# Kernel optimization log

Hardware: AMD Instinct MI355X
Metric: run time of the kernel (lower is better)

Reference implementation:

```python
import jax, jax.numpy as jnp
import numpy as np

N = 100000       # num_nodes
E = 800000       # num edges (avg degree 8)
EMB = 64         # emb_dim
HID = 256        # hidden_dim


def setup_inputs() -> dict:
    key = jax.random.key(0)
    k1, k2, k3, k4, k5, k6, k7 = jax.random.split(key, 7)
    def xavier(k, fan_in, fan_out):
        limit = float(np.sqrt(6.0 / (fan_in + fan_out)))
        return jax.random.uniform(k, (fan_in, fan_out), jnp.float32, -limit, limit)
    return {
        "row": jax.random.randint(k1, (E,), 0, N, dtype=jnp.int64) if jax.config.jax_enable_x64 else jax.random.randint(k1, (E,), 0, N).astype(jnp.int32),
        "col": jax.random.randint(k2, (E,), 0, N).astype(jnp.int32),
        "val": jax.random.uniform(k3, (E,), jnp.float32),
        "emb": jax.random.normal(k4, (N, EMB), jnp.float32) * 0.02,
        "W0": xavier(k5, EMB, HID),
        "W1": xavier(k6, HID, HID),
        "W2": xavier(k7, HID, HID),
    }


def reference(row, col, val, emb, W0, W1, W2):
    # SpMM: out[r] = sum_{edges e with row[e]==r} val[e] * emb[col[e]]
    msgs = val[:, None] * emb[col]                      # [E, EMB] gather + scale
    x = jax.ops.segment_sum(msgs, row, num_segments=N)  # [N, EMB] scatter-add
    # MLP (bias-free linears; dropout=0.0 / eval mode => identity)
    x = jax.nn.relu(x @ W0)   # [N, HID]
    x = jax.nn.relu(x @ W1)   # [N, HID]
    x = x @ W2                # [N, HID]
    return x
```

## Files before the change

### kernel.cpp

```cpp
#include <hip/hip_runtime.h>
#include <hip/hip_bf16.h>

#define EMB 64
#define HID 256

typedef __attribute__((ext_vector_type(8))) short short8_t;
typedef __attribute__((ext_vector_type(4))) float f32x4;

__device__ __forceinline__ unsigned short f2bf(float f)
{
    union { float f; unsigned int u; } c; c.f = f;
    unsigned int u = c.u;
    u += 0x7fffu + ((u >> 16) & 1u);
    return (unsigned short)(u >> 16);
}
__device__ __forceinline__ float bf2f(unsigned short b)
{
    union { unsigned int u; float f; } c; c.u = ((unsigned int)b) << 16;
    return c.f;
}

__global__ __launch_bounds__(256) void prep_kernel(
    const float* __restrict__ emb, const float* __restrict__ W0,
    const float* __restrict__ W1, const float* __restrict__ W2,
    int* __restrict__ counts, unsigned short* __restrict__ embb,
    unsigned short* __restrict__ W0t, unsigned short* __restrict__ W1t,
    unsigned short* __restrict__ W2t, int M, int zb, int cb)
{
    int b = blockIdx.x;
    if (b < zb) {
        int idx = (b * 256 + threadIdx.x) * 4;
        if (idx + 3 < M) {
            int4 z; z.x = 0; z.y = 0; z.z = 0; z.w = 0;
            *(int4*)&counts[idx] = z;
        } else {
            for (int i = idx; i < M; ++i) counts[i] = 0;
        }
        return;
    }
    b -= zb;
    if (b < cb) {
        int idx = (b * 256 + threadIdx.x) * 4;
        if (idx + 3 < M * EMB) {
            float4 v = *(const float4*)&emb[idx];
            ushort4 o;
            o.x = f2bf(v.x); o.y = f2bf(v.y); o.z = f2bf(v.z); o.w = f2bf(v.w);
            *(ushort4*)&embb[idx] = o;
        }
        return;
    }
    b -= cb;
    if (b < EMB) {
        int i = b * 256 + threadIdx.x;
        int k = i >> 8, n = i & 255;
        W0t[n * EMB + k] = f2bf(W0[i]);
        return;
    }
    b -= EMB;
    if (b < HID) {
        int i = b * 256 + threadIdx.x;
        int k = i >> 8, n = i & 255;
        W1t[n * HID + k] = f2bf(W1[i]);
        return;
    }
    b -= HID;
    {
        int i = b * 256 + threadIdx.x;
        int k = i >> 8, n = i & 255;
        W2t[n * HID + k] = f2bf(W2[i]);
    }
}

__global__ __launch_bounds__(256) void hist_kernel(
    const int* __restrict__ row, int* __restrict__ counts, int E)
{
    int base = (blockIdx.x * 256 + threadIdx.x) * 4;
    if (base + 3 < E) {
        int4 r4 = *(const int4*)&row[base];
        atomicAdd(&counts[r4.x], 1);
        atomicAdd(&counts[r4.y], 1);
        atomicAdd(&counts[r4.z], 1);
        atomicAdd(&counts[r4.w], 1);
    } else {
        for (int i = base; i < E; ++i) atomicAdd(&counts[row[i]], 1);
    }
}

__global__ __launch_bounds__(256) void scan_phase1(
    const int* __restrict__ counts, int* __restrict__ excl,
    int* __restrict__ blockSums, int n)
{
    __shared__ int s[256];
    int t = threadIdx.x;
    int base = blockIdx.x * 1024 + t * 4;
    int4 v = {0, 0, 0, 0};
    if (base + 3 < n) {
        v = *(const int4*)&counts[base];
    } else {
        if (base + 0 < n) v.x = counts[base + 0];
        if (base + 1 < n) v.y = counts[base + 1];
        if (base + 2 < n) v.z = counts[base + 2];
        if (base + 3 < n) v.w = counts[base + 3];
    }
    int tsum = v.x + v.y + v.z + v.w;
    s[t] = tsum;
    __syncthreads();
#pragma unroll
    for (int off = 1; off < 256; off <<= 1) {
        int val = (t >= off) ? s[t - off] : 0;
        __syncthreads();
        s[t] += val;
        __syncthreads();
    }
    if (t == 255) blockSums[blockIdx.x] = s[255];
    int e0 = s[t] - tsum;
    int e1 = e0 + v.x;
    int e2 = e1 + v.y;
    int e3 = e2 + v.z;
    if (base + 0 < n) excl[base + 0] = e0;
    if (base + 1 < n) excl[base + 1] = e1;
    if (base + 2 < n) excl[base + 2] = e2;
    if (base + 3 < n) excl[base + 3] = e3;
}

__global__ __launch_bounds__(256) void scan_phase2(int* blockSums, int nb)
{
    __shared__ int s[256];
    int t = threadIdx.x;
    int v = (t < nb) ? blockSums[t] : 0;
    s[t] = v;
    __syncthreads();
#pragma unroll
    for (int off = 1; off < 256; off <<= 1) {
        int val = (t >= off) ? s[t - off] : 0;
        __syncthreads();
        s[t] += val;
        __syncthreads();
    }
    if (t < nb) blockSums[t] = s[t] - v;
}

__global__ __launch_bounds__(256) void scan_phase3(
    int* __restrict__ offsets, const int* __restrict__ blockSums,
    int* __restrict__ cursor, int n)
{
    int i = blockIdx.x * 256 + threadIdx.x;
    if (i >= n) return;
    int o = offsets[i] + blockSums[i >> 10];
    offsets[i] = o;
    cursor[i]  = o;
}

__global__ __launch_bounds__(256) void scatter_kernel(
    const int* __restrict__ row, const int* __restrict__ col,
    const float* __restrict__ val, int* __restrict__ cursor,
    uint2* __restrict__ edata, int E)
{
    int e = blockIdx.x * 256 + threadIdx.x;
    if (e >= E) return;
    int r = row[e];
    int pos = atomicAdd(&cursor[r], 1);
    uint2 d;
    d.x = (unsigned)col[e];
    d.y = __float_as_uint(val[e]);
    edata[pos] = d;
}

__global__ __launch_bounds__(256) void pull_kernel(
    const int* __restrict__ offsets, const int* __restrict__ counts,
    const uint2* __restrict__ edata, const unsigned short* __restrict__ embb,
    unsigned short* __restrict__ xb, int Nn)
{
    int r    = blockIdx.x * 4 + (threadIdx.x >> 6);
    int lane = threadIdx.x & 63;
    if (r >= Nn) return;
    int beg = offsets[r];
    int cnt = counts[r];
    float acc = 0.f;
    for (int i = 0; i < cnt; i += 8) {
        uint2 ed[8];
#pragma unroll
        for (int j = 0; j < 8; ++j) {
            int idx = i + j;
            idx = (idx < cnt) ? idx : (cnt - 1);
            ed[j] = edata[beg + idx];
        }
        float g[8];
#pragma unroll
        for (int j = 0; j < 8; ++j)
            g[j] = bf2f(embb[(size_t)ed[j].x * EMB + lane]);
#pragma unroll
        for (int j = 0; j < 8; ++j) {
            float v = (i + j < cnt) ? __uint_as_float(ed[j].y) : 0.f;
            acc += v * g[j];
        }
    }
    xb[(size_t)r * EMB + lane] = f2bf(acc);
}

__global__ __launch_bounds__(256) void mlp_fused(
    const unsigned short* __restrict__ xb,
    const unsigned short* __restrict__ W0t,
    const unsigned short* __restrict__ W1t,
    const unsigned short* __restrict__ W2t,
    float* __restrict__ out, int M)
{
    constexpr int LDK = 72;
    constexpr int LDH = 264;
    __shared__ unsigned short As[64 * LDK];
    __shared__ unsigned short Bs[256 * LDK];
    __shared__ unsigned short H [64 * LDH];

    const int t    = threadIdx.x;
    const int lane = t & 63;
    const int w    = t >> 6;
    const int lr   = lane & 15;
    const int kg   = lane >> 4;
    const int row0 = blockIdx.x * 64;

#pragma unroll
    for (int c = 0; c < 2; ++c) {
        int chunk = t + c * 256;
        int r = chunk >> 3, ko = (chunk & 7) * 8;
        int gr = row0 + r;
        *(short8_t*)&As[r * LDK + ko] =
            *(const short8_t*)(xb + (size_t)(gr < M ? gr : 0) * EMB + ko);
    }
#pragma unroll
    for (int c = 0; c < 8; ++c) {
        int chunk = t + c * 256;
        int n = chunk >> 3, ko = (chunk & 7) * 8;
        *(short8_t*)&Bs[n * LDK + ko] = *(const short8_t*)(W0t + n * EMB + ko);
    }
    __syncthreads();

    f32x4 acc[4][4] = {};
#pragma unroll
    for (int ks = 0; ks < 64; ks += 32) {
        short8_t a[4], b[4];
#pragma unroll
        for (int m = 0; m < 4; ++m)
            a[m] = *(const short8_t*)&As[(m * 16 + lr) * LDK + ks + kg * 8];
#pragma unroll
        for (int n = 0; n < 4; ++n)
            b[n] = *(const short8_t*)&Bs[(w * 64 + n * 16 + lr) * LDK + ks + kg * 8];
#pragma unroll
        for (int m = 0; m < 4; ++m)
#pragma unroll
            for (int n = 0; n < 4; ++n)
                acc[m][n] = __builtin_amdgcn_mfma_f32_16x16x32_bf16(
                    a[m], b[n], acc[m][n], 0, 0, 0);
    }
#pragma unroll
    for (int m = 0; m < 4; ++m)
#pragma unroll
        for (int r = 0; r < 4; ++r)
#pragma unroll
            for (int n = 0; n < 4; ++n)
                H[(m * 16 + kg * 4 + r) * LDH + w * 64 + n * 16 + lr] =
                    f2bf(fmaxf(acc[m][n][r], 0.f));
    __syncthreads();

    f32x4 acc2[4][4] = {};
    for (int k0 = 0; k0 < HID; k0 += 64) {
#pragma unroll
        for (int c = 0; c < 8; ++c) {
            int chunk = t + c * 256;
            int n = chunk >> 3, ko = (chunk & 7) * 8;
            *(short8_t*)&Bs[n * LDK + ko] =
                *(const short8_t*)(W1t + (size_t)n * HID + k0 + ko);
        }
        __syncthreads();
#pragma unroll
        for (int ks = 0; ks < 64; ks += 32) {
            short8_t a[4], b[4];
#pragma unroll
            for (int m = 0; m < 4; ++m)
                a[m] = *(const short8_t*)&H[(m * 16 + lr) * LDH + k0 + ks + kg * 8];
#pragma unroll
            for (int n = 0; n < 4; ++n)
                b[n] = *(const short8_t*)&Bs[(w * 64 + n * 16 + lr) * LDK + ks + kg * 8];
#pragma unroll
            for (int m = 0; m < 4; ++m)
#pragma unroll
                for (int n = 0; n < 4; ++n)
                    acc2[m][n] = __builtin_amdgcn_mfma_f32_16x16x32_bf16(
                        a[m], b[n], acc2[m][n], 0, 0, 0);
        }
        __syncthreads();
    }
#pragma unroll
    for (int m = 0; m < 4; ++m)
#pragma unroll
        for (int r = 0; r < 4; ++r)
#pragma unroll
            for (int n = 0; n < 4; ++n)
                H[(m * 16 + kg * 4 + r) * LDH + w * 64 + n * 16 + lr] =
                    f2bf(fmaxf(acc2[m][n][r], 0.f));

    f32x4 acc3[4][4] = {};
    for (int k0 = 0; k0 < HID; k0 += 64) {
#pragma unroll
        for (int c = 0; c < 8; ++c) {
            int chunk = t + c * 256;
            int n = chunk >> 3, ko = (chunk & 7) * 8;
            *(short8_t*)&Bs[n * LDK + ko] =
                *(const short8_t*)(W2t + (size_t)n * HID + k0 + ko);
        }
        __syncthreads();
#pragma unroll
        for (int ks = 0; ks < 64; ks += 32) {
            short8_t a[4], b[4];
#pragma unroll
            for (int m = 0; m < 4; ++m)
                a[m] = *(const short8_t*)&H[(m * 16 + lr) * LDH + k0 + ks + kg * 8];
#pragma unroll
            for (int n = 0; n < 4; ++n)
                b[n] = *(const short8_t*)&Bs[(w * 64 + n * 16 + lr) * LDK + ks + kg * 8];
#pragma unroll
            for (int m = 0; m < 4; ++m)
#pragma unroll
                for (int n = 0; n < 4; ++n)
                    acc3[m][n] = __builtin_amdgcn_mfma_f32_16x16x32_bf16(
                        a[m], b[n], acc3[m][n], 0, 0, 0);
        }
        __syncthreads();
    }
#pragma unroll
    for (int m = 0; m < 4; ++m)
#pragma unroll
        for (int r = 0; r < 4; ++r) {
            int gr = row0 + m * 16 + kg * 4 + r;
            if (gr < M)
#pragma unroll
                for (int n = 0; n < 4; ++n)
                    out[(size_t)gr * HID + w * 64 + n * 16 + lr] = acc3[m][n][r];
        }
}

__global__ __launch_bounds__(256) void spmm_kernel(
    const int* __restrict__ row, const int* __restrict__ col,
    const float* __restrict__ val, const float* __restrict__ emb,
    float* __restrict__ x, int E)
{
    int gid  = blockIdx.x * blockDim.x + threadIdx.x;
    int e    = gid >> 6;
    int lane = gid & 63;
    if (e >= E) return;
    unsafeAtomicAdd(&x[(size_t)row[e] * EMB + lane],
                    val[e] * emb[(size_t)col[e] * EMB + lane]);
}

template<int K, bool RELU>
__global__ __launch_bounds__(256) void gemm_f32(
    const float* A, const float* __restrict__ B, float* C, int M)
{
    __shared__ float As[64][17];
    __shared__ float Bs[16][256];

    const int t    = threadIdx.x;
    const int tn   = t & 15;
    const int row0 = blockIdx.x * 64;
    const int sk = t & 15;
    const int sm = (t >> 4) * 4;

    float acc[4][16];
#pragma unroll
    for (int i = 0; i < 4; ++i)
#pragma unroll
        for (int j = 0; j < 16; ++j) acc[i][j] = 0.f;

    const int mB = ((t & 63) >> 4) * 4;
    const int wq = t >> 6;
    const int myM = (wq * 16) + mB;

    for (int k0 = 0; k0 < K; k0 += 16) {
        __syncthreads();
#pragma unroll
        for (int i = 0; i < 4; ++i) {
            int m  = sm + i;
            int gr = row0 + m;
            As[m][sk] = (gr < M) ? A[(size_t)gr * K + k0 + sk] : 0.f;
        }
#pragma unroll
        for (int r = 0; r < 16; ++r)
            Bs[r][t] = B[(size_t)(k0 + r) * 256 + t];
        __syncthreads();

#pragma unroll
        for (int kk = 0; kk < 16; ++kk) {
            float a0 = As[myM + 0][kk];
            float a1 = As[myM + 1][kk];
            float a2 = As[myM + 2][kk];
            float a3 = As[myM + 3][kk];
            float4 b[4];
#pragma unroll
            for (int j = 0; j < 4; ++j)
                b[j] = *(const float4*)&Bs[kk][tn * 4 + j * 64];
#pragma unroll
            for (int j = 0; j < 4; ++j) {
                acc[0][j*4+0] += a0 * b[j].x;  acc[0][j*4+1] += a0 * b[j].y;
                acc[0][j*4+2] += a0 * b[j].z;  acc[0][j*4+3] += a0 * b[j].w;
                acc[1][j*4+0] += a1 * b[j].x;  acc[1][j*4+1] += a1 * b[j].y;
                acc[1][j*4+2] += a1 * b[j].z;  acc[1][j*4+3] += a1 * b[j].w;
                acc[2][j*4+0] += a2 * b[j].x;  acc[2][j*4+1] += a2 * b[j].y;
                acc[2][j*4+2] += a2 * b[j].z;  acc[2][j*4+3] += a2 * b[j].w;
                acc[3][j*4+0] += a3 * b[j].x;  acc[3][j*4+1] += a3 * b[j].y;
                acc[3][j*4+2] += a3 * b[j].z;  acc[3][j*4+3] += a3 * b[j].w;
            }
        }
    }

#pragma unroll
    for (int i = 0; i < 4; ++i) {
        int gr = row0 + myM + i;
        if (gr < M) {
#pragma unroll
            for (int j = 0; j < 4; ++j) {
                float4 o;
                o.x = acc[i][j*4+0]; o.y = acc[i][j*4+1];
                o.z = acc[i][j*4+2]; o.w = acc[i][j*4+3];
                if (RELU) {
                    o.x = fmaxf(o.x, 0.f); o.y = fmaxf(o.y, 0.f);
                    o.z = fmaxf(o.z, 0.f); o.w = fmaxf(o.w, 0.f);
                }
                *(float4*)&C[(size_t)gr * 256 + tn * 4 + j * 64] = o;
            }
        }
    }
}

extern "C" void kernel_launch(void* const* d_in, const int* in_sizes, int n_in,
                              void* d_out, int out_size, void* d_ws, size_t ws_size,
                              hipStream_t stream)
{
    const int*   row = (const int*)d_in[0];
    const int*   col = (const int*)d_in[1];
    const float* val = (const float*)d_in[2];
    const float* emb = (const float*)d_in[3];
    const float* W0  = (const float*)d_in[4];
    const float* W1  = (const float*)d_in[5];
    const float* W2  = (const float*)d_in[6];
    float* out = (float*)d_out;

    const int E = in_sizes[0];
    const int M = in_sizes[3] / EMB;

    char* ws = (char*)d_ws;

    size_t off = 0;
    auto alloc = [&](size_t bytes) { size_t o = off; off = (off + bytes + 255) & ~(size_t)255; return o; };
    const size_t off_counts = alloc((size_t)M * 4);
    const size_t off_offs   = alloc((size_t)M * 4);
    const size_t off_cursor = alloc((size_t)M * 4);
    const size_t off_bsums  = alloc(1024);
    const size_t off_edata  = alloc((size_t)E * 8);
    const size_t off_embb   = alloc((size_t)M * EMB * 2);
    const size_t off_xb     = alloc((size_t)M * EMB * 2);
    const size_t off_w0     = alloc((size_t)EMB * HID * 2);
    const size_t off_w1     = alloc((size_t)HID * HID * 2);
    const size_t off_w2     = alloc((size_t)HID * HID * 2);
    const size_t need       = off;

    int gblocks = (M + 63) / 64;

    if (ws_size >= need) {
        int*   counts = (int*)(ws + off_counts);
        int*   offs   = (int*)(ws + off_offs);
        int*   cursor = (int*)(ws + off_cursor);
        int*   bsums  = (int*)(ws + off_bsums);
        uint2* edata  = (uint2*)(ws + off_edata);
        unsigned short* embb = (unsigned short*)(ws + off_embb);
        unsigned short* xb  = (unsigned short*)(ws + off_xb);
        unsigned short* W0t = (unsigned short*)(ws + off_w0);
        unsigned short* W1t = (unsigned short*)(ws + off_w1);
        unsigned short* W2t = (unsigned short*)(ws + off_w2);

        int zb = (M / 4 + 255) / 256;
        int cb = ((M * EMB) / 4 + 255) / 256;
        int prep_blocks = zb + cb + EMB + HID + HID;
        prep_kernel<<<prep_blocks, 256, 0, stream>>>(
            emb, W0, W1, W2, counts, embb, W0t, W1t, W2t, M, zb, cb);

        hist_kernel<<<(E / 4 + 255) / 256, 256, 0, stream>>>(row, counts, E);
        int nb = (M + 1023) / 1024;
        scan_phase1<<<nb, 256, 0, stream>>>(counts, offs, bsums, M);
        scan_phase2<<<1, 256, 0, stream>>>(bsums, nb);
        scan_phase3<<<(M + 255) / 256, 256, 0, stream>>>(offs, bsums, cursor, M);
        scatter_kernel<<<(E + 255) / 256, 256, 0, stream>>>(row, col, val, cursor, edata, E);

        pull_kernel<<<(M + 3) / 4, 256, 0, stream>>>(offs, counts, edata, embb, xb, M);

        mlp_fused<<<gblocks, 256, 0, stream>>>(xb, W0t, W1t, W2t, out, M);
    } else {
        float* x = (float*)ws;
        (void)hipMemsetAsync(x, 0, (size_t)M * EMB * sizeof(float), stream);
        spmm_kernel<<<(E + 3) / 4, 256, 0, stream>>>(row, col, val, emb, x, E);
        gemm_f32<EMB, true ><<<gblocks, 256, 0, stream>>>(x,   W0, out, M);
        gemm_f32<HID, true ><<<gblocks, 256, 0, stream>>>(out, W1, out, M);
        gemm_f32<HID, false><<<gblocks, 256, 0, stream>>>(out, W2, out, M);
    }
}
```

Before: 203.6 us.

## Double-buffer weight tiles with register prefetch in fused MLP kernel

Restructures the fused three-layer MLP kernel to stage weight K-slices of 32 through two shared-memory buffers, with global loads prefetched into registers one step ahead. This overlaps weight fetches with MFMA work and halves the barriers per K step. The input activations are loaded straight into registers, so the As tile goes away. Shared memory use drops, which may allow more blocks per CU, at the cost of more live registers for the prefetch staging.

```diff
diff --git a/kernel.cpp b/kernel.cpp
--- a/kernel.cpp
+++ b/kernel.cpp
@@ -205,10 +205,9 @@
     const unsigned short* __restrict__ W2t,
     float* __restrict__ out, int M)
 {
-    constexpr int LDK = 72;
+    constexpr int LDK = 40;
     constexpr int LDH = 264;
-    __shared__ unsigned short As[64 * LDK];
-    __shared__ unsigned short Bs[256 * LDK];
+    __shared__ unsigned short Bs[2][256 * LDK];
     __shared__ unsigned short H [64 * LDH];
 
     const int t    = threadIdx.x;
@@ -218,38 +217,52 @@
     const int kg   = lane >> 4;
     const int row0 = blockIdx.x * 64;
 
-#pragma unroll
-    for (int c = 0; c < 2; ++c) {
-        int chunk = t + c * 256;
-        int r = chunk >> 3, ko = (chunk & 7) * 8;
-        int gr = row0 + r;
-        *(short8_t*)&As[r * LDK + ko] =
-            *(const short8_t*)(xb + (size_t)(gr < M ? gr : 0) * EMB + ko);
-    }
-#pragma unroll
-    for (int c = 0; c < 8; ++c) {
-        int chunk = t + c * 256;
-        int n = chunk >> 3, ko = (chunk & 7) * 8;
-        *(short8_t*)&Bs[n * LDK + ko] = *(const short8_t*)(W0t + n * EMB + ko);
-    }
+    const int srow = t >> 2;
+    const int sq   = (t & 3) * 8;
+
+    short8_t st[4];
+#define LOADC(src, ldk, k0)                                                    \
+    do {                                                                       \
+        _Pragma("unroll")                                                      \
+        for (int c = 0; c < 4; ++c)                                            \
+            st[c] = *(const short8_t*)((src) + (size_t)(64 * c + srow) * (ldk) \
+                                       + (k0) + sq);                           \
+    } while (0)
+#define WRITEC(buf)                                                            \
+    do {                                                                       \
+        _Pragma("unroll")                                                      \
+        for (int c = 0; c < 4; ++c)                                            \
+            *(short8_t*)&Bs[buf][(64 * c + srow) * LDK + sq] = st[c];          \
+    } while (0)
+
+    short8_t ax[2][4];
+#pragma unroll
+    for (int h = 0; h < 2; ++h)
+#pragma unroll
+        for (int m = 0; m < 4; ++m) {
+            int gr = row0 + m * 16 + lr;
+            ax[h][m] = *(const short8_t*)(xb + (size_t)(gr < M ? gr : 0) * EMB
+                                          + h * 32 + kg * 8);
+        }
+
+    LOADC(W0t, EMB, 0);  WRITEC(0);
+    LOADC(W0t, EMB, 32); WRITEC(1);
     __syncthreads();
+    LOADC(W1t, HID, 0);
 
     f32x4 acc[4][4] = {};
 #pragma unroll
-    for (int ks = 0; ks < 64; ks += 32) {
-        short8_t a[4], b[4];
-#pragma unroll
-        for (int m = 0; m < 4; ++m)
-            a[m] = *(const short8_t*)&As[(m * 16 + lr) * LDK + ks + kg * 8];
+    for (int h = 0; h < 2; ++h) {
+        short8_t b[4];
 #pragma unroll
         for (int n = 0; n < 4; ++n)
-            b[n] = *(const short8_t*)&Bs[(w * 64 + n * 16 + lr) * LDK + ks + kg * 8];
+            b[n] = *(const short8_t*)&Bs[h][(w * 64 + n * 16 + lr) * LDK + kg * 8];
 #pragma unroll
         for (int m = 0; m < 4; ++m)
 #pragma unroll
             for (int n = 0; n < 4; ++n)
                 acc[m][n] = __builtin_amdgcn_mfma_f32_16x16x32_bf16(
-                    a[m], b[n], acc[m][n], 0, 0, 0);
+                    ax[h][m], b[n], acc[m][n], 0, 0, 0);
     }
 #pragma unroll
     for (int m = 0; m < 4; ++m)
@@ -261,31 +274,33 @@
                     f2bf(fmaxf(acc[m][n][r], 0.f));
     __syncthreads();
 
+    WRITEC(0);
+    LOADC(W1t, HID, 32);
+    __syncthreads();
+
     f32x4 acc2[4][4] = {};
-    for (int k0 = 0; k0 < HID; k0 += 64) {
-#pragma unroll
-        for (int c = 0; c < 8; ++c) {
-            int chunk = t + c * 256;
-            int n = chunk >> 3, ko = (chunk & 7) * 8;
-            *(short8_t*)&Bs[n * LDK + ko] =
-                *(const short8_t*)(W1t + (size_t)n * HID + k0 + ko);
-        }
-        __syncthreads();
-#pragma unroll
-        for (int ks = 0; ks < 64; ks += 32) {
-            short8_t a[4], b[4];
-#pragma unroll
-            for (int m = 0; m < 4; ++m)
-                a[m] = *(const short8_t*)&H[(m * 16 + lr) * LDH + k0 + ks + kg * 8];
+    for (int i = 0; i < 8; ++i) {
+        int cur = i & 1;
+        short8_t a[4], b[4];
+#pragma unroll
+        for (int m = 0; m < 4; ++m)
+            a[m] = *(const short8_t*)&H[(m * 16 + lr) * LDH + i * 32 + kg * 8];
+#pragma unroll
+        for (int n = 0; n < 4; ++n)
+            b[n] = *(const short8_t*)&Bs[cur][(w * 64 + n * 16 + lr) * LDK + kg * 8];
+#pragma unroll
+        for (int m = 0; m < 4; ++m)
 #pragma unroll
             for (int n = 0; n < 4; ++n)
-                b[n] = *(const short8_t*)&Bs[(w * 64 + n * 16 + lr) * LDK + ks + kg * 8];
-#pragma unroll
-            for (int m = 0; m < 4; ++m)
-#pragma unroll
-                for (int n = 0; n < 4; ++n)
-                    acc2[m][n] = __builtin_amdgcn_mfma_f32_16x16x32_bf16(
-                        a[m], b[n], acc2[m][n], 0, 0, 0);
+                acc2[m][n] = __builtin_amdgcn_mfma_f32_16x16x32_bf16(
+                    a[m], b[n], acc2[m][n], 0, 0, 0);
+        WRITEC(cur ^ 1);
+        if (i < 6) {
+            LOADC(W1t, HID, (i + 2) * 32);
+        } else if (i == 6) {
+            LOADC(W2t, HID, 0);
+        } else {
+            LOADC(W2t, HID, 32);
         }
         __syncthreads();
     }
@@ -297,34 +312,31 @@
             for (int n = 0; n < 4; ++n)
                 H[(m * 16 + kg * 4 + r) * LDH + w * 64 + n * 16 + lr] =
                     f2bf(fmaxf(acc2[m][n][r], 0.f));
+    __syncthreads();
 
     f32x4 acc3[4][4] = {};
-    for (int k0 = 0; k0 < HID; k0 += 64) {
-#pragma unroll
-        for (int c = 0; c < 8; ++c) {
-            int chunk = t + c * 256;
-            int n = chunk >> 3, ko = (chunk & 7) * 8;
-            *(short8_t*)&Bs[n * LDK + ko] =
-                *(const short8_t*)(W2t + (size_t)n * HID + k0 + ko);
-        }
-        __syncthreads();
-#pragma unroll
-        for (int ks = 0; ks < 64; ks += 32) {
-            short8_t a[4], b[4];
-#pragma unroll
-            for (int m = 0; m < 4; ++m)
-                a[m] = *(const short8_t*)&H[(m * 16 + lr) * LDH + k0 + ks + kg * 8];
+    for (int i = 0; i < 8; ++i) {
+        int cur = i & 1;
+        short8_t a[4], b[4];
+#pragma unroll
+        for (int m = 0; m < 4; ++m)
+            a[m] = *(const short8_t*)&H[(m * 16 + lr) * LDH + i * 32 + kg * 8];
+#pragma unroll
+        for (int n = 0; n < 4; ++n)
+            b[n] = *(const short8_t*)&Bs[cur][(w * 64 + n * 16 + lr) * LDK + kg * 8];
+#pragma unroll
+        for (int m = 0; m < 4; ++m)
 #pragma unroll
             for (int n = 0; n < 4; ++n)
-                b[n] = *(const short8_t*)&Bs[(w * 64 + n * 16 + lr) * LDK + ks + kg * 8];
-#pragma unroll
-            for (int m = 0; m < 4; ++m)
-#pragma unroll
-                for (int n = 0; n < 4; ++n)
-                    acc3[m][n] = __builtin_amdgcn_mfma_f32_16x16x32_bf16(
-                        a[m], b[n], acc3[m][n], 0, 0, 0);
-        }
-        __syncthreads();
+                acc3[m][n] = __builtin_amdgcn_mfma_f32_16x16x32_bf16(
+                    a[m], b[n], acc3[m][n], 0, 0, 0);
+        if (i < 7) {
+            WRITEC(cur ^ 1);
+            if (i < 6) {
+                LOADC(W2t, HID, (i + 2) * 32);
+            }
+            __syncthreads();
+        }
     }
 #pragma unroll
     for (int m = 0; m < 4; ++m)
@@ -336,6 +348,8 @@
                 for (int n = 0; n < 4; ++n)
                     out[(size_t)gr * HID + w * 64 + n * 16 + lr] = acc3[m][n][r];
         }
+#undef LOADC
+#undef WRITEC
 }
 
 __global__ __launch_bounds__(256) void spmm_kernel(
```

New measurement: 201.3 us. No clear change (-1.1%).

## Pre-swizzle weights into MFMA fragment order and read B operands straight from global

Applied to the files above, without the earlier changes.

The weight prep now writes W0/W1/W2 in per-lane MFMA fragment order, so the fused MLP loads B operands directly from global/L2 with one 16-byte load per lane and no longer stages them through shared memory. The first-layer A operand is also read directly from global into registers. The hidden activation buffer uses an XOR-swizzled unpadded layout to avoid LDS bank conflicts. Together these remove most __syncthreads and LDS traffic and cut LDS usage, which may raise occupancy, at the cost of every block re-reading weights from L2.

```diff
diff --git a/kernel.cpp b/kernel.cpp
--- a/kernel.cpp
+++ b/kernel.cpp
@@ -24,8 +24,8 @@
     const float* __restrict__ emb, const float* __restrict__ W0,
     const float* __restrict__ W1, const float* __restrict__ W2,
     int* __restrict__ counts, unsigned short* __restrict__ embb,
-    unsigned short* __restrict__ W0t, unsigned short* __restrict__ W1t,
-    unsigned short* __restrict__ W2t, int M, int zb, int cb)
+    unsigned short* __restrict__ W0f, unsigned short* __restrict__ W1f,
+    unsigned short* __restrict__ W2f, int M, int zb, int cb)
 {
     int b = blockIdx.x;
     if (b < zb) {
@@ -50,24 +50,45 @@
         return;
     }
     b -= cb;
-    if (b < EMB) {
-        int i = b * 256 + threadIdx.x;
-        int k = i >> 8, n = i & 255;
-        W0t[n * EMB + k] = f2bf(W0[i]);
+    if (b < 8) {
+        int i    = b * 256 + threadIdx.x;
+        int lane = i & 63;
+        int kc   = (i >> 6) & 1;
+        int nt   = i >> 7;
+        int lr   = lane & 15, kg = lane >> 4;
+        unsigned short tmp[8];
+#pragma unroll
+        for (int j = 0; j < 8; ++j)
+            tmp[j] = f2bf(W0[(kc * 32 + kg * 8 + j) * HID + nt * 16 + lr]);
+        *(short8_t*)&W0f[(size_t)i * 8] = *(short8_t*)tmp;
         return;
     }
-    b -= EMB;
-    if (b < HID) {
-        int i = b * 256 + threadIdx.x;
-        int k = i >> 8, n = i & 255;
-        W1t[n * HID + k] = f2bf(W1[i]);
+    b -= 8;
+    if (b < 32) {
+        int i    = b * 256 + threadIdx.x;
+        int lane = i & 63;
+        int kc   = (i >> 6) & 7;
+        int nt   = i >> 9;
+        int lr   = lane & 15, kg = lane >> 4;
+        unsigned short tmp[8];
+#pragma unroll
+        for (int j = 0; j < 8; ++j)
+            tmp[j] = f2bf(W1[(kc * 32 + kg * 8 + j) * HID + nt * 16 + lr]);
+        *(short8_t*)&W1f[(size_t)i * 8] = *(short8_t*)tmp;
         return;
     }
-    b -= HID;
+    b -= 32;
     {
-        int i = b * 256 + threadIdx.x;
-        int k = i >> 8, n = i & 255;
-        W2t[n * HID + k] = f2bf(W2[i]);
+        int i    = b * 256 + threadIdx.x;
+        int lane = i & 63;
+        int kc   = (i >> 6) & 7;
+        int nt   = i >> 9;
+        int lr   = lane & 15, kg = lane >> 4;
+        unsigned short tmp[8];
+#pragma unroll
+        for (int j = 0; j < 8; ++j)
+            tmp[j] = f2bf(W2[(kc * 32 + kg * 8 + j) * HID + nt * 16 + lr]);
+        *(short8_t*)&W2f[(size_t)i * 8] = *(short8_t*)tmp;
     }
 }
 
@@ -200,16 +221,12 @@
 
 __global__ __launch_bounds__(256) void mlp_fused(
     const unsigned short* __restrict__ xb,
-    const unsigned short* __restrict__ W0t,
-    const unsigned short* __restrict__ W1t,
-    const unsigned short* __restrict__ W2t,
+    const unsigned short* __restrict__ W0f,
+    const unsigned short* __restrict__ W1f,
+    const unsigned short* __restrict__ W2f,
     float* __restrict__ out, int M)
 {
-    constexpr int LDK = 72;
-    constexpr int LDH = 264;
-    __shared__ unsigned short As[64 * LDK];
-    __shared__ unsigned short Bs[256 * LDK];
-    __shared__ unsigned short H [64 * LDH];
+    __shared__ unsigned short H[64 * 256];
 
     const int t    = threadIdx.x;
     const int lane = t & 63;
@@ -217,39 +234,32 @@
     const int lr   = lane & 15;
     const int kg   = lane >> 4;
     const int row0 = blockIdx.x * 64;
-
-#pragma unroll
-    for (int c = 0; c < 2; ++c) {
-        int chunk = t + c * 256;
-        int r = chunk >> 3, ko = (chunk & 7) * 8;
-        int gr = row0 + r;
-        *(short8_t*)&As[r * LDK + ko] =
-            *(const short8_t*)(xb + (size_t)(gr < M ? gr : 0) * EMB + ko);
-    }
-#pragma unroll
-    for (int c = 0; c < 8; ++c) {
-        int chunk = t + c * 256;
-        int n = chunk >> 3, ko = (chunk & 7) * 8;
-        *(short8_t*)&Bs[n * LDK + ko] = *(const short8_t*)(W0t + n * EMB + ko);
-    }
-    __syncthreads();
-
+    char* Hb = (char*)H;
+
+#define HOFF(row, bytecol) ((((row) * 512) + (bytecol)) ^ (((row) & 7) << 4))
+
+    short8_t ax[2][4];
+#pragma unroll
+    for (int kc = 0; kc < 2; ++kc)
+#pragma unroll
+        for (int m = 0; m < 4; ++m) {
+            int gr = row0 + m * 16 + lr;
+            ax[kc][m] = *(const short8_t*)(xb + (size_t)(gr < M ? gr : 0) * EMB
+                                           + kc * 32 + kg * 8);
+        }
     f32x4 acc[4][4] = {};
 #pragma unroll
-    for (int ks = 0; ks < 64; ks += 32) {
-        short8_t a[4], b[4];
-#pragma unroll
-        for (int m = 0; m < 4; ++m)
-            a[m] = *(const short8_t*)&As[(m * 16 + lr) * LDK + ks + kg * 8];
+    for (int kc = 0; kc < 2; ++kc) {
+        short8_t b[4];
 #pragma unroll
         for (int n = 0; n < 4; ++n)
-            b[n] = *(const short8_t*)&Bs[(w * 64 + n * 16 + lr) * LDK + ks + kg * 8];
+            b[n] = *(const short8_t*)&W0f[(size_t)(((w * 4 + n) * 2 + kc) * 64 + lane) * 8];
 #pragma unroll
         for (int m = 0; m < 4; ++m)
 #pragma unroll
             for (int n = 0; n < 4; ++n)
                 acc[m][n] = __builtin_amdgcn_mfma_f32_16x16x32_bf16(
-                    a[m], b[n], acc[m][n], 0, 0, 0);
+                    ax[kc][m], b[n], acc[m][n], 0, 0, 0);
     }
 #pragma unroll
     for (int m = 0; m < 4; ++m)
@@ -257,74 +267,56 @@
         for (int r = 0; r < 4; ++r)
 #pragma unroll
             for (int n = 0; n < 4; ++n)
-                H[(m * 16 + kg * 4 + r) * LDH + w * 64 + n * 16 + lr] =
+                *(unsigned short*)(Hb + HOFF(m * 16 + kg * 4 + r,
+                                             (w * 64 + n * 16 + lr) * 2)) =
                     f2bf(fmaxf(acc[m][n][r], 0.f));
     __syncthreads();
 
     f32x4 acc2[4][4] = {};
-    for (int k0 = 0; k0 < HID; k0 += 64) {
-#pragma unroll
-        for (int c = 0; c < 8; ++c) {
-            int chunk = t + c * 256;
-            int n = chunk >> 3, ko = (chunk & 7) * 8;
-            *(short8_t*)&Bs[n * LDK + ko] =
-                *(const short8_t*)(W1t + (size_t)n * HID + k0 + ko);
-        }
-        __syncthreads();
-#pragma unroll
-        for (int ks = 0; ks < 64; ks += 32) {
-            short8_t a[4], b[4];
-#pragma unroll
-            for (int m = 0; m < 4; ++m)
-                a[m] = *(const short8_t*)&H[(m * 16 + lr) * LDH + k0 + ks + kg * 8];
+#pragma unroll
+    for (int kc = 0; kc < 8; ++kc) {
+        short8_t a[4], b[4];
+#pragma unroll
+        for (int n = 0; n < 4; ++n)
+            b[n] = *(const short8_t*)&W1f[(size_t)(((w * 4 + n) * 8 + kc) * 64 + lane) * 8];
+#pragma unroll
+        for (int m = 0; m < 4; ++m)
+            a[m] = *(const short8_t*)(Hb + HOFF(m * 16 + lr, kc * 64 + kg * 16));
+#pragma unroll
+        for (int m = 0; m < 4; ++m)
 #pragma unroll
             for (int n = 0; n < 4; ++n)
-                b[n] = *(const short8_t*)&Bs[(w * 64 + n * 16 + lr) * LDK + ks + kg * 8];
-#pragma unroll
-            for (int m = 0; m < 4; ++m)
-#pragma unroll
-                for (int n = 0; n < 4; ++n)
-                    acc2[m][n] = __builtin_amdgcn_mfma_f32_16x16x32_bf16(
-                        a[m], b[n], acc2[m][n], 0, 0, 0);
-        }
-        __syncthreads();
-    }
+                acc2[m][n] = __builtin_amdgcn_mfma_f32_16x16x32_bf16(
+                    a[m], b[n], acc2[m][n], 0, 0, 0);
+    }
+    __syncthreads();
 #pragma unroll
     for (int m = 0; m < 4; ++m)
 #pragma unroll
         for (int r = 0; r < 4; ++r)
 #pragma unroll
             for (int n = 0; n < 4; ++n)
-                H[(m * 16 + kg * 4 + r) * LDH + w * 64 + n * 16 + lr] =
+                *(unsigned short*)(Hb + HOFF(m * 16 + kg * 4 + r,
+                                             (w * 64 + n * 16 + lr) * 2)) =
                     f2bf(fmaxf(acc2[m][n][r], 0.f));
+    __syncthreads();
 
     f32x4 acc3[4][4] = {};
-    for (int k0 = 0; k0 < HID; k0 += 64) {
-#pragma unroll
-        for (int c = 0; c < 8; ++c) {
-            int chunk = t + c * 256;
-            int n = chunk >> 3, ko = (chunk & 7) * 8;
-            *(short8_t*)&Bs[n * LDK + ko] =
-                *(const short8_t*)(W2t + (size_t)n * HID + k0 + ko);
-        }
-        __syncthreads();
-#pragma unroll
-        for (int ks = 0; ks < 64; ks += 32) {
-            short8_t a[4], b[4];
-#pragma unroll
-            for (int m = 0; m < 4; ++m)
-                a[m] = *(const short8_t*)&H[(m * 16 + lr) * LDH + k0 + ks + kg * 8];
+#pragma unroll
+    for (int kc = 0; kc < 8; ++kc) {
+        short8_t a[4], b[4];
+#pragma unroll
+        for (int n = 0; n < 4; ++n)
+            b[n] = *(const short8_t*)&W2f[(size_t)(((w * 4 + n) * 8 + kc) * 64 + lane) * 8];
+#pragma unroll
+        for (int m = 0; m < 4; ++m)
+            a[m] = *(const short8_t*)(Hb + HOFF(m * 16 + lr, kc * 64 + kg * 16));
+#pragma unroll
+        for (int m = 0; m < 4; ++m)
 #pragma unroll
             for (int n = 0; n < 4; ++n)
-                b[n] = *(const short8_t*)&Bs[(w * 64 + n * 16 + lr) * LDK + ks + kg * 8];
-#pragma unroll
-            for (int m = 0; m < 4; ++m)
-#pragma unroll
-                for (int n = 0; n < 4; ++n)
-                    acc3[m][n] = __builtin_amdgcn_mfma_f32_16x16x32_bf16(
-                        a[m], b[n], acc3[m][n], 0, 0, 0);
-        }
-        __syncthreads();
+                acc3[m][n] = __builtin_amdgcn_mfma_f32_16x16x32_bf16(
+                    a[m], b[n], acc3[m][n], 0, 0, 0);
     }
 #pragma unroll
     for (int m = 0; m < 4; ++m)
@@ -336,6 +328,7 @@
                 for (int n = 0; n < 4; ++n)
                     out[(size_t)gr * HID + w * 64 + n * 16 + lr] = acc3[m][n][r];
         }
+#undef HOFF
 }
 
 __global__ __launch_bounds__(256) void spmm_kernel(
@@ -472,15 +465,15 @@
         uint2* edata  = (uint2*)(ws + off_edata);
         unsigned short* embb = (unsigned short*)(ws + off_embb);
         unsigned short* xb  = (unsigned short*)(ws + off_xb);
-        unsigned short* W0t = (unsigned short*)(ws + off_w0);
-        unsigned short* W1t = (unsigned short*)(ws + off_w1);
-        unsigned short* W2t = (unsigned short*)(ws + off_w2);
+        unsigned short* W0f = (unsigned short*)(ws + off_w0);
+        unsigned short* W1f = (unsigned short*)(ws + off_w1);
+        unsigned short* W2f = (unsigned short*)(ws + off_w2);
 
         int zb = (M / 4 + 255) / 256;
         int cb = ((M * EMB) / 4 + 255) / 256;
-        int prep_blocks = zb + cb + EMB + HID + HID;
+        int prep_blocks = zb + cb + 8 + 32 + 32;
         prep_kernel<<<prep_blocks, 256, 0, stream>>>(
-            emb, W0, W1, W2, counts, embb, W0t, W1t, W2t, M, zb, cb);
+            emb, W0, W1, W2, counts, embb, W0f, W1f, W2f, M, zb, cb);
 
         hist_kernel<<<(E / 4 + 255) / 256, 256, 0, stream>>>(row, counts, E);
         int nb = (M + 1023) / 1024;
@@ -491,7 +484,7 @@
 
         pull_kernel<<<(M + 3) / 4, 256, 0, stream>>>(offs, counts, edata, embb, xb, M);
 
-        mlp_fused<<<gblocks, 256, 0, stream>>>(xb, W0t, W1t, W2t, out, M);
+        mlp_fused<<<gblocks, 256, 0, stream>>>(xb, W0f, W1f, W2f, out, M);
     } else {
         float* x = (float*)ws;
         (void)hipMemsetAsync(x, 0, (size_t)M * EMB * sizeof(float), stream);
```

Measured after the change: 201.0 us. Within noise of the previous version (-1.3%).
